# Kernel tuning notes

Measured on AMD Instinct MI355X. Metric: run time of the kernel, lower is better.

Reference implementation:

```python
import jax, jax.numpy as jnp
import numpy as np

NODES = 23   # 22 players + ball per frame-graph
K = 8        # random neighbors per node
B, T = 64, 128
G = B * T            # total graphs (frames)
N = G * NODES        # total nodes
D_IN, H, RH = 16, 128, 128


def setup_inputs() -> dict:
    key = jax.random.key(0)
    ks = jax.random.split(key, 10)
    x = jax.random.normal(ks[0], (N, D_IN), jnp.float32)
    # per-graph random edges: dst = each node repeated K times, src = random node in same graph
    src_local = jax.random.randint(ks[1], (G, NODES * K), 0, NODES)
    dst_local = jnp.tile(jnp.repeat(jnp.arange(NODES), K)[None, :], (G, 1))
    off = (jnp.arange(G) * NODES)[:, None]
    edge_index = jnp.stack([(src_local + off).reshape(-1),
                            (dst_local + off).reshape(-1)]).astype(jnp.int32)
    runner_idx = jax.random.randint(ks[2], (G,), 0, NODES, dtype=jnp.int32)
    sc = lambda k, sh: (jax.random.normal(k, sh, jnp.float32) * 0.05)
    return {
        'x': x, 'edge_index': edge_index, 'runner_idx': runner_idx,
        'W1': sc(ks[3], (D_IN, H)), 'b1': jnp.zeros((H,), jnp.float32),
        'W2': sc(ks[4], (H, H)),    'b2': jnp.zeros((H,), jnp.float32),
        'W_ih': sc(ks[5], (3 * RH, H)), 'W_hh': sc(ks[6], (3 * RH, RH)),
        'b_ih': jnp.zeros((3 * RH,), jnp.float32), 'b_hh': jnp.zeros((3 * RH,), jnp.float32),
        'Wp': sc(ks[7], (RH, 2)), 'bp': jnp.zeros((2,), jnp.float32),
    }


def _gcn_conv(h, edge_index, W, b):
    # PyG GCNConv: add self-loops, symmetric normalization, scatter-sum
    h = h @ W
    loop = jnp.arange(N, dtype=edge_index.dtype)
    s = jnp.concatenate([edge_index[0], loop])
    d = jnp.concatenate([edge_index[1], loop])
    deg = jax.ops.segment_sum(jnp.ones_like(s, h.dtype), d, num_segments=N)
    dinv = jnp.where(deg > 0, jax.lax.rsqrt(deg), 0.0)
    norm = dinv[s] * dinv[d]                      # [E+N]
    out = jax.ops.segment_sum(h[s] * norm[:, None], d, num_segments=N)
    return out + b


def _gru(seq, W_ih, W_hh, b_ih, b_hh):
    # torch GRU: gates in r,z,n order
    xg = seq @ W_ih.T + b_ih                      # [B,T,3RH]
    def step(hprev, xt):
        gh = hprev @ W_hh.T + b_hh
        xr, xz, xn = jnp.split(xt, 3, axis=-1)
        hr, hz, hn = jnp.split(gh, 3, axis=-1)
        r = jax.nn.sigmoid(xr + hr)
        z = jax.nn.sigmoid(xz + hz)
        n = jnp.tanh(xn + r * hn)
        hnew = (1.0 - z) * n + z * hprev
        return hnew, hnew
    h0 = jnp.zeros((seq.shape[0], RH), seq.dtype)
    _, outs = jax.lax.scan(step, h0, jnp.swapaxes(xg, 0, 1))
    return jnp.swapaxes(outs, 0, 1)               # [B,T,RH]


def reference(x, edge_index, runner_idx, W1, b1, W2, b2,
              W_ih, W_hh, b_ih, b_hh, Wp, bp):
    h = jax.nn.relu(_gcn_conv(x, edge_index, W1, b1))
    h = jax.nn.relu(_gcn_conv(h, edge_index, W2, b2))
    # fused equivalent of the per-graph nonzero()/indexing loop:
    runner_global = jnp.arange(G, dtype=jnp.int32) * NODES + runner_idx
    seq = h[runner_global].reshape(B, T, H)       # all lengths == T, padding is a no-op
    out = _gru(seq, W_ih, W_hh, b_ih, b_hh)
    return out @ Wp + bp                          # [B,T,2]
```

## Files before the change

### kernel.cpp

```cpp
#include <hip/hip_runtime.h>
#include <hip/hip_bf16.h>
#include <math.h>

#define GG 8192
#define NODESN 23
#define KK 8
#define DIN 16
#define HH 128
#define RHH 128
#define EPG (NODESN*KK)
#define TTT 128
#define BBB 64

#define GRU_BARRIER() asm volatile("s_waitcnt lgkmcnt(0)\n\ts_barrier" ::: "memory")

__global__ __launch_bounds__(256) void gcn_hsum(
    const float* __restrict__ x, const int* __restrict__ esrc,
    const int* __restrict__ runner,
    const float* __restrict__ W1, const float* __restrict__ b1,
    float* __restrict__ hsum_g)
{
    __shared__ float xs[NODESN * DIN];
    __shared__ int   srcs[EPG];
    __shared__ float t1[NODESN * HH];
    __shared__ float red[256];

    const int g   = blockIdx.x;
    const int tid = threadIdx.x;
    const int j   = tid & 127;
    const int nh  = tid >> 7;

    for (int i = tid; i < NODESN * DIN; i += 256) xs[i] = x[g * NODESN * DIN + i];
    for (int i = tid; i < EPG; i += 256)          srcs[i] = esrc[g * EPG + i] - g * NODESN;

    float w[DIN];
    #pragma unroll
    for (int k = 0; k < DIN; k++) w[k] = W1[k * HH + j];
    const float b1j = b1[j];
    __syncthreads();

    const int n0 = nh * 12;
    const int n1 = nh ? NODESN : 12;
    for (int n = n0; n < n1; n++) {
        float acc = 0.f;
        #pragma unroll
        for (int k = 0; k < DIN; k += 4) {
            float4 xv = *(const float4*)&xs[n * DIN + k];
            acc = fmaf(xv.x, w[k], fmaf(xv.y, w[k+1], fmaf(xv.z, w[k+2], fmaf(xv.w, w[k+3], acc))));
        }
        t1[n * HH + j] = acc;
    }
    __syncthreads();

    const int r = runner[g];
    float part = 0.f;
    for (int slot = nh; slot < 9; slot += 2) {
        int node = (slot < 8) ? srcs[r * KK + slot] : r;
        float acc = t1[node * HH + j];
        #pragma unroll
        for (int k = 0; k < KK; k++) acc += t1[srcs[node * KK + k] * HH + j];
        part += fmaxf(acc * (1.f / 9.f) + b1j, 0.f);
    }
    red[tid] = part;
    __syncthreads();
    if (tid < HH) hsum_g[(size_t)g * HH + tid] = red[tid] + red[tid + 128];
}

__global__ __launch_bounds__(256) void seq_kernel(
    const float* __restrict__ hsum_g, const float* __restrict__ W2,
    const float* __restrict__ b2, float* __restrict__ seq)
{
    __shared__ float hs[16 * HH];
    const int tid = threadIdx.x;
    const int j = tid & 127, mh = tid >> 7;
    const size_t base = (size_t)blockIdx.x * 16 * HH;

    for (int v = tid; v < 16 * HH / 4; v += 256)
        ((float4*)hs)[v] = ((const float4*)(hsum_g + base))[v];
    __syncthreads();

    float acc[8];
    #pragma unroll
    for (int m = 0; m < 8; m++) acc[m] = 0.f;
    const float* hrow = hs + mh * 8 * HH;
    for (int k = 0; k < HH; k += 4) {
        float w0  = W2[(k+0)*HH + j];
        float w1  = W2[(k+1)*HH + j];
        float w2v = W2[(k+2)*HH + j];
        float w3  = W2[(k+3)*HH + j];
        #pragma unroll
        for (int m = 0; m < 8; m++) {
            float4 hv = *(const float4*)&hrow[m * HH + k];
            acc[m] = fmaf(hv.x, w0, fmaf(hv.y, w1, fmaf(hv.z, w2v, fmaf(hv.w, w3, acc[m]))));
        }
    }
    const float bj = b2[j];
    #pragma unroll
    for (int m = 0; m < 8; m++)
        seq[base + (size_t)(mh * 8 + m) * HH + j] = fmaxf(acc[m] * (1.f/9.f) + bj, 0.f);
}

__global__ void transpose_wih(const float* __restrict__ W, float* __restrict__ WT)
{
    int idx = blockIdx.x * 256 + threadIdx.x;
    if (idx < 3 * RHH * RHH) {
        int jj = idx / RHH, kk = idx - jj * RHH;
        WT[kk * (3 * RHH) + jj] = W[idx];
    }
}

__global__ __launch_bounds__(384) void xg_kernel(
    const float* __restrict__ seq, const float* __restrict__ WT,
    const float* __restrict__ b_ih, float* __restrict__ xg)
{
    const int tid = threadIdx.x;
    const int m0 = blockIdx.x * 8;
    const float* srow = seq + (size_t)m0 * RHH;
    float acc[8];
    const float bv = b_ih[tid];
    #pragma unroll
    for (int mi = 0; mi < 8; mi++) acc[mi] = bv;
    for (int k = 0; k < RHH; k += 4) {
        float w0 = WT[(k+0)*384 + tid];
        float w1 = WT[(k+1)*384 + tid];
        float w2 = WT[(k+2)*384 + tid];
        float w3 = WT[(k+3)*384 + tid];
        #pragma unroll
        for (int mi = 0; mi < 8; mi++) {
            float4 sv = *(const float4*)(srow + mi * RHH + k);
            acc[mi] = fmaf(sv.x, w0, fmaf(sv.y, w1, fmaf(sv.z, w2, fmaf(sv.w, w3, acc[mi]))));
        }
    }
    #pragma unroll
    for (int mi = 0; mi < 8; mi++)
        xg[(size_t)(m0 + mi) * 384 + tid] = acc[mi];
}

__global__ __launch_bounds__(1024)
__attribute__((amdgpu_waves_per_eu(4, 4)))
void gru_kernel(
    const float* __restrict__ xg, const float* __restrict__ W_hh,
    const float* __restrict__ b_hh, float* __restrict__ h_out)
{
    __shared__ float hbuf[2][HH];
    __shared__ float xg_s[2][3 * RHH];

    const int b   = blockIdx.x;
    const int tid = threadIdx.x;
    const int i   = tid >> 3;
    const int q   = tid & 7;

    float wr[16], wz[16], wn[16];
    int loff[4];
    {
        const float* br = W_hh + (size_t)i * RHH;
        const float* bz = br + (size_t)RHH * RHH;
        const float* bn = bz + (size_t)RHH * RHH;
        #pragma unroll
        for (int m = 0; m < 4; m++) {
            int p = (m + (q >> 1)) & 3;
            int o = q * 16 + 4 * p;
            loff[m] = o;
            float4 v;
            v = *(const float4*)(br + o); wr[4*m]=v.x; wr[4*m+1]=v.y; wr[4*m+2]=v.z; wr[4*m+3]=v.w;
            v = *(const float4*)(bz + o); wz[4*m]=v.x; wz[4*m+1]=v.y; wz[4*m+2]=v.z; wz[4*m+3]=v.w;
            v = *(const float4*)(bn + o); wn[4*m]=v.x; wn[4*m+1]=v.y; wn[4*m+2]=v.z; wn[4*m+3]=v.w;
        }
    }

    float bhr = 0.f, bhz = 0.f, bhn = 0.f;
    if (q == 0) { bhr = b_hh[i]; bhz = b_hh[RHH + i]; bhn = b_hh[2 * RHH + i]; }

    if (tid < HH) hbuf[0][tid] = 0.f;
    const float* xbase = xg + (size_t)b * TTT * 3 * RHH;
    float xnext = 0.f;
    if (tid < 3 * RHH) {
        xg_s[0][tid] = xbase[tid];
        xnext = xbase[3 * RHH + tid];
    }
    float hprev = 0.f;
    float* hob = h_out + (size_t)b * TTT * HH;
    __syncthreads();

    for (int t = 0; t < TTT; t++) {
        const float* hrow = hbuf[t & 1];
        float ar = 0.f, az = 0.f, an = 0.f;
        #pragma unroll
        for (int m = 0; m < 4; m++) {
            float4 hv = *(const float4*)(hrow + loff[m]);
            ar = fmaf(hv.x, wr[4*m], fmaf(hv.y, wr[4*m+1], fmaf(hv.z, wr[4*m+2], fmaf(hv.w, wr[4*m+3], ar))));
            az = fmaf(hv.x, wz[4*m], fmaf(hv.y, wz[4*m+1], fmaf(hv.z, wz[4*m+2], fmaf(hv.w, wz[4*m+3], az))));
            an = fmaf(hv.x, wn[4*m], fmaf(hv.y, wn[4*m+1], fmaf(hv.z, wn[4*m+2], fmaf(hv.w, wn[4*m+3], an))));
        }

        if (tid < 3 * RHH) {
            xg_s[(t + 1) & 1][tid] = xnext;
            xnext = (t + 2 < TTT) ? xbase[(size_t)(t + 2) * 3 * RHH + tid] : 0.f;
        }

        ar += __shfl_xor(ar, 1); ar += __shfl_xor(ar, 2); ar += __shfl_xor(ar, 4);
        az += __shfl_xor(az, 1); az += __shfl_xor(az, 2); az += __shfl_xor(az, 4);
        an += __shfl_xor(an, 1); an += __shfl_xor(an, 2); an += __shfl_xor(an, 4);

        if (q == 0) {
            const float* xr_s = xg_s[t & 1];
            float xr = xr_s[i], xz = xr_s[RHH + i], xn = xr_s[2 * RHH + i];
            float sr = xr + ar + bhr;
            float sz = xz + az + bhz;
            float rg = 1.f / (1.f + __expf(-sr));
            float zg = 1.f / (1.f + __expf(-sz));
            float tv = fmaf(rg, an + bhn, xn);
            tv = fminf(fmaxf(tv, -15.f), 15.f);
            float e2 = __expf(-2.f * tv);
            float ng = (1.f - e2) / (1.f + e2);
            hprev = fmaf(zg, hprev, (1.f - zg) * ng);
            hbuf[(t + 1) & 1][i] = hprev;
            hob[t * HH + i] = hprev;
        }
        GRU_BARRIER();
    }
}

__global__ __launch_bounds__(256) void proj_kernel(
    const float* __restrict__ h_out, const float* __restrict__ Wp,
    const float* __restrict__ bp, float* __restrict__ out)
{
    __shared__ float wps[2 * RHH];
    __shared__ float bps[2];
    const int tid = threadIdx.x;
    if (tid < 2 * RHH) wps[tid] = Wp[tid];
    if (tid < 2) bps[tid] = bp[tid];
    __syncthreads();

    const int s = tid & 7;
    const int rl = tid >> 3;
    const size_t row = (size_t)blockIdx.x * 32 + rl;
    const float* hr = h_out + row * HH + s * 16;
    float a0 = 0.f, a1 = 0.f;
    #pragma unroll
    for (int m = 0; m < 16; m += 4) {
        float4 hv = *(const float4*)(hr + m);
        int k = s * 16 + m;
        a0 = fmaf(hv.x, wps[(k+0)*2], fmaf(hv.y, wps[(k+1)*2], fmaf(hv.z, wps[(k+2)*2], fmaf(hv.w, wps[(k+3)*2], a0))));
        a1 = fmaf(hv.x, wps[(k+0)*2+1], fmaf(hv.y, wps[(k+1)*2+1], fmaf(hv.z, wps[(k+2)*2+1], fmaf(hv.w, wps[(k+3)*2+1], a1))));
    }
    a0 += __shfl_xor(a0, 1); a0 += __shfl_xor(a0, 2); a0 += __shfl_xor(a0, 4);
    a1 += __shfl_xor(a1, 1); a1 += __shfl_xor(a1, 2); a1 += __shfl_xor(a1, 4);
    if (s == 0) {
        out[row * 2 + 0] = a0 + bps[0];
        out[row * 2 + 1] = a1 + bps[1];
    }
}

extern "C" void kernel_launch(void* const* d_in, const int* in_sizes, int n_in,
                              void* d_out, int out_size, void* d_ws, size_t ws_size,
                              hipStream_t stream)
{
    const float* x      = (const float*)d_in[0];
    const int*   eidx   = (const int*)d_in[1];
    const int*   runner = (const int*)d_in[2];
    const float* W1     = (const float*)d_in[3];
    const float* b1     = (const float*)d_in[4];
    const float* W2     = (const float*)d_in[5];
    const float* b2     = (const float*)d_in[6];
    const float* W_ih   = (const float*)d_in[7];
    const float* W_hh   = (const float*)d_in[8];
    const float* b_ih   = (const float*)d_in[9];
    const float* b_hh   = (const float*)d_in[10];
    const float* Wp     = (const float*)d_in[11];
    const float* bp     = (const float*)d_in[12];
    float* out = (float*)d_out;

    float* seq    = (float*)d_ws;
    float* xg     = seq + (size_t)GG * HH;
    float* WT     = xg + (size_t)GG * 3 * RHH;
    float* hsum_g = xg;
    float* h_out  = seq;

    transpose_wih<<<192, 256, 0, stream>>>(W_ih, WT);
    gcn_hsum<<<GG, 256, 0, stream>>>(x, eidx, runner, W1, b1, hsum_g);
    seq_kernel<<<GG / 16, 256, 0, stream>>>(hsum_g, W2, b2, seq);
    xg_kernel<<<GG / 8, 384, 0, stream>>>(seq, WT, b_ih, xg);
    gru_kernel<<<BBB, 1024, 0, stream>>>(xg, W_hh, b_hh, h_out);
    proj_kernel<<<GG / 32, 256, 0, stream>>>(h_out, Wp, bp, out);
}
```

Measured before the change: 280.3 us.

## Remap GRU thread layout so all lanes compute gates redundantly

Changes the GRU kernel's thread-to-row mapping so that the 8 partial-dot lanes for a hidden unit are strided by 8 within a wavefront, reducing with xor shuffles of 8/16/32. All lanes now compute the gate nonlinearities redundantly, and only q==0 writes, which removes the divergent branch. The LDS bank-swizzle offset is adjusted and a large static shared buffer (about 81KB) is declared, apparently to cap occupancy at one block per CU. The custom waitcnt+barrier asm is replaced by __syncthreads.

```diff
diff --git a/kernel.cpp b/kernel.cpp
--- a/kernel.cpp
+++ b/kernel.cpp
@@ -12,8 +12,6 @@
 #define TTT 128
 #define BBB 64
 
-#define GRU_BARRIER() asm volatile("s_waitcnt lgkmcnt(0)\n\ts_barrier" ::: "memory")
-
 __global__ __launch_bounds__(256) void gcn_hsum(
     const float* __restrict__ x, const int* __restrict__ esrc,
     const int* __restrict__ runner,
@@ -136,19 +134,25 @@
         xg[(size_t)(m0 + mi) * 384 + tid] = acc[mi];
 }
 
+#define SMEM_FLOATS 20736
+#define XG0 0
+#define HB0 768
+
 __global__ __launch_bounds__(1024)
 __attribute__((amdgpu_waves_per_eu(4, 4)))
 void gru_kernel(
     const float* __restrict__ xg, const float* __restrict__ W_hh,
     const float* __restrict__ b_hh, float* __restrict__ h_out)
 {
-    __shared__ float hbuf[2][HH];
-    __shared__ float xg_s[2][3 * RHH];
-
-    const int b   = blockIdx.x;
-    const int tid = threadIdx.x;
-    const int i   = tid >> 3;
-    const int q   = tid & 7;
+    __shared__ float smem[SMEM_FLOATS];
+
+    const int b    = blockIdx.x;
+    const int tid  = threadIdx.x;
+    const int lane = tid & 63;
+    const int q    = lane >> 3;
+    const int i    = ((tid >> 6) << 3) | (lane & 7);
+
+    if (tid == 0) smem[SMEM_FLOATS - 1] = 0.f;
 
     float wr[16], wz[16], wn[16];
     int loff[4];
@@ -158,7 +162,7 @@
         const float* bn = bz + (size_t)RHH * RHH;
         #pragma unroll
         for (int m = 0; m < 4; m++) {
-            int p = (m + (q >> 1)) & 3;
+            int p = (m + q) & 3;
             int o = q * 16 + 4 * p;
             loff[m] = o;
             float4 v;
@@ -168,14 +172,15 @@
         }
     }
 
-    float bhr = 0.f, bhz = 0.f, bhn = 0.f;
-    if (q == 0) { bhr = b_hh[i]; bhz = b_hh[RHH + i]; bhn = b_hh[2 * RHH + i]; }
-
-    if (tid < HH) hbuf[0][tid] = 0.f;
+    const float bhr = b_hh[i];
+    const float bhz = b_hh[RHH + i];
+    const float bhn = b_hh[2 * RHH + i];
+
+    if (tid < HH) smem[HB0 + tid] = 0.f;
     const float* xbase = xg + (size_t)b * TTT * 3 * RHH;
     float xnext = 0.f;
     if (tid < 3 * RHH) {
-        xg_s[0][tid] = xbase[tid];
+        smem[XG0 + tid] = xbase[tid];
         xnext = xbase[3 * RHH + tid];
     }
     float hprev = 0.f;
@@ -183,7 +188,7 @@
     __syncthreads();
 
     for (int t = 0; t < TTT; t++) {
-        const float* hrow = hbuf[t & 1];
+        const float* hrow = &smem[HB0 + ((t & 1) << 7)];
         float ar = 0.f, az = 0.f, an = 0.f;
         #pragma unroll
         for (int m = 0; m < 4; m++) {
@@ -194,16 +199,16 @@
         }
 
         if (tid < 3 * RHH) {
-            xg_s[(t + 1) & 1][tid] = xnext;
+            smem[XG0 + (((t + 1) & 1) * 3 * RHH) + tid] = xnext;
             xnext = (t + 2 < TTT) ? xbase[(size_t)(t + 2) * 3 * RHH + tid] : 0.f;
         }
 
-        ar += __shfl_xor(ar, 1); ar += __shfl_xor(ar, 2); ar += __shfl_xor(ar, 4);
-        az += __shfl_xor(az, 1); az += __shfl_xor(az, 2); az += __shfl_xor(az, 4);
-        an += __shfl_xor(an, 1); an += __shfl_xor(an, 2); an += __shfl_xor(an, 4);
-
-        if (q == 0) {
-            const float* xr_s = xg_s[t & 1];
+        ar += __shfl_xor(ar, 8); ar += __shfl_xor(ar, 16); ar += __shfl_xor(ar, 32);
+        az += __shfl_xor(az, 8); az += __shfl_xor(az, 16); az += __shfl_xor(az, 32);
+        an += __shfl_xor(an, 8); an += __shfl_xor(an, 16); an += __shfl_xor(an, 32);
+
+        {
+            const float* xr_s = &smem[XG0 + ((t & 1) * 3 * RHH)];
             float xr = xr_s[i], xz = xr_s[RHH + i], xn = xr_s[2 * RHH + i];
             float sr = xr + ar + bhr;
             float sz = xz + az + bhz;
@@ -214,10 +219,12 @@
             float e2 = __expf(-2.f * tv);
             float ng = (1.f - e2) / (1.f + e2);
             hprev = fmaf(zg, hprev, (1.f - zg) * ng);
-            hbuf[(t + 1) & 1][i] = hprev;
-            hob[t * HH + i] = hprev;
-        }
-        GRU_BARRIER();
+            if (q == 0) {
+                smem[HB0 + (((t + 1) & 1) << 7) + i] = hprev;
+                hob[t * HH + i] = hprev;
+            }
+        }
+        __syncthreads();
     }
 }
 
```

Result: no change. 276.3 us (-1.4%).
